# Optimization experiments

Measured on AMD Instinct MI355X. Metric: run time of the kernel, lower is better.

## Reference

```python
import jax, jax.numpy as jnp
import numpy as np

# Quantum circuit math: each wire starts in |0>, gets RX(x_i) (encoder), then a
# single-qubit, the n-wire state is a product state and each wire's <Z> is
# analytically cos(theta_i) * cos(x_i):
#   RX(x)|0> = [cos(x/2), -i sin(x/2)];  after RY(th):
#   <Z> = (cos^2(th/2)-sin^2(th/2)) * (cos^2(x/2)-sin^2(x/2)) = cos(th)cos(x).
# This is exactly the math the torchquantum simulator computes, expressed in
# closed form (no 2^d_k state vector needed).

NUM_HEADS = 64


def setup_inputs() -> dict:
    key = jax.random.key(0)
    k1, k2, k3 = jax.random.split(key, 3)
    B, T, E = 4, 1024, 512
    d_k = E // NUM_HEADS  # 8 wires
    x = jax.random.normal(k1, (B, T, E), dtype=jnp.float32)
    theta = jax.random.normal(k2, (d_k,), dtype=jnp.float32)  # shared RY params (one QLayer reused across heads)
    W_combine = jax.random.normal(k3, (E, E), dtype=jnp.float32) * (E ** -0.5)
    b_combine = jnp.zeros((E,), dtype=jnp.float32)
    return {"x": x, "theta": theta, "W_combine": W_combine, "b_combine": b_combine}


def reference(x, theta, W_combine, b_combine):
    B, T, E = x.shape
    H = NUM_HEADS
    d_k = E // H
    # split heads: [B, H, T, d_k]
    xh = x.reshape(B, T, H, d_k).transpose(0, 2, 1, 3)
    # quantum layer output: per-wire PauliZ expectation = cos(theta) * cos(x)
    proj = jnp.cos(xh) * jnp.cos(theta)  # [B, H, T, d_k]
    # self-attention on quantum projections
    scale = 1.0 / (d_k ** 0.5)
    scores = jnp.einsum('bhtd,bhsd->bhts', proj, proj) * scale  # [B, H, T, T]
    probs = jax.nn.softmax(scores, axis=-1)
    # dropout is identity in eval mode
    attn = jnp.einsum('bhts,bhsd->bhtd', probs, proj)  # [B, H, T, d_k]
    out = attn.transpose(0, 2, 1, 3).reshape(B, T, E)
    return out @ W_combine.T + b_combine
```

## Files before the change

### kernel.cpp

```cpp
#include <hip/hip_runtime.h>
#include <hip/hip_bf16.h>
#include <cstdint>
#include <cstddef>

#define T_DIM 1024
#define E_DIM 512

typedef short bf16x8 __attribute__((ext_vector_type(8)));
typedef float f32x4  __attribute__((ext_vector_type(4)));

__global__ __launch_bounds__(1024)
void qattn_mfma(const float* __restrict__ x,
                const float* __restrict__ theta,
                const float* __restrict__ W,
                __hip_bfloat16* __restrict__ attn_out,
                __hip_bfloat16* __restrict__ w_bf)
{
    __shared__ __align__(16) char shraw[16384 + 20640];
    auto projA = (__hip_bfloat16 (*)[8])(shraw);
    auto projT = (__hip_bfloat16 (*)[1032])(shraw + 16384);

    const int head = blockIdx.x;
    const int b    = head >> 6;
    const int h    = head & 63;
    const int tid  = threadIdx.x;
    const int lane = tid & 63;
    const int wv   = tid >> 6;
    const int rlo  = lane & 15;
    const int quad = lane >> 4;

    {
        const int gid = head * 1024 + tid;
        if (gid < 65536) {
            const float4 v = *(const float4*)(W + gid * 4);
            alignas(8) __hip_bfloat16 ob[4] = {
                __float2bfloat16(v.x), __float2bfloat16(v.y),
                __float2bfloat16(v.z), __float2bfloat16(v.w)};
            *(uint2*)(w_bf + gid * 4) = *(const uint2*)ob;
        }
    }

    const float SA2 = 8.0804315f;
    float ctT[8], ctA[8];
#pragma unroll
    for (int d = 0; d < 8; ++d) {
        ctT[d] = __cosf(theta[d]);
        ctA[d] = ctT[d] * SA2;
    }

    const float* xb = x + (size_t)b * T_DIM * E_DIM + h * 8;
    {
        const int r = tid;
        const float4 v0 = *(const float4*)(xb + (size_t)r * E_DIM);
        const float4 v1 = *(const float4*)(xb + (size_t)r * E_DIM + 4);
        float pr[8] = {v0.x, v0.y, v0.z, v0.w, v1.x, v1.y, v1.z, v1.w};
        alignas(16) __hip_bfloat16 ra[8];
#pragma unroll
        for (int d = 0; d < 8; ++d) {
            const float c = __cosf(pr[d]);
            ra[d] = __float2bfloat16(c * ctA[d]);
            projT[d][r] = __float2bfloat16(c * ctT[d]);
        }
        *(uint4*)&projA[r][0] = *(const uint4*)ra;
        projT[8][r] = __ushort_as_bfloat16((unsigned short)0x3f80);
        projT[9][r] = __ushort_as_bfloat16((unsigned short)0);
    }
    __syncthreads();

    const bf16x8 z8 = {};

    const float MAGIC = 8404858.0f;
    const f32x4 cinit = {MAGIC, MAGIC, MAGIC, MAGIC};

    const int q0 = wv * 64;
    bf16x8 bq[4];
#pragma unroll
    for (int tl = 0; tl < 4; ++tl)
        bq[tl] = (quad == 0) ? *(const bf16x8*)&projA[q0 + tl * 16 + rlo][0]
                             : z8;

    f32x4 nacc[4] = {};

    const __hip_bfloat16* kabase =
        (quad == 0) ? &projA[rlo][0] : &projA[0][0];
    const int bvrow = (rlo < 8) ? rlo : ((rlo == 8) ? 8 : 9);
    const __hip_bfloat16* bvbase = &projT[bvrow][quad * 4];

#pragma unroll
    for (int kc = 0; kc < 32; ++kc) {
        const int key0 = kc * 32;
        const bf16x8 ka0 = *(const bf16x8*)(kabase + (size_t)key0 * 8);
        const bf16x8 ka1 = *(const bf16x8*)(kabase + (size_t)(key0 + 16) * 8);
        union { uint2 u[2]; bf16x8 v; } uu;
        uu.u[0] = *(const uint2*)(bvbase + key0);
        uu.u[1] = *(const uint2*)(bvbase + key0 + 16);
        const bf16x8 bv = uu.v;

        f32x4 s0[4], s1[4];
#pragma unroll
        for (int tl = 0; tl < 4; ++tl) {
            s0[tl] = __builtin_amdgcn_mfma_f32_16x16x32_bf16(
                ka0, bq[tl], cinit, 0, 0, 0);
            s1[tl] = __builtin_amdgcn_mfma_f32_16x16x32_bf16(
                ka1, bq[tl], cinit, 0, 0, 0);
        }

#pragma unroll
        for (int tl = 0; tl < 4; ++tl) {
            union { f32x4 f; uint32_t u[4]; } a0, a1;
            a0.f = s0[tl];
            a1.f = s1[tl];
            union { uint32_t u[4]; bf16x8 v; } pk;
            pk.u[0] = __builtin_amdgcn_perm(a0.u[1], a0.u[0], 0x05040100u);
            pk.u[1] = __builtin_amdgcn_perm(a0.u[3], a0.u[2], 0x05040100u);
            pk.u[2] = __builtin_amdgcn_perm(a1.u[1], a1.u[0], 0x05040100u);
            pk.u[3] = __builtin_amdgcn_perm(a1.u[3], a1.u[2], 0x05040100u);
            nacc[tl] = __builtin_amdgcn_mfma_f32_16x16x32_bf16(
                pk.v, bv, nacc[tl], 0, 0, 0);
        }
    }

    const int denSrc = (lane & 48) | 8;
#pragma unroll
    for (int tl = 0; tl < 4; ++tl) {
#pragma unroll
        for (int r = 0; r < 4; ++r) {
            const float den = __shfl(nacc[tl][r], denSrc);
            const float inv = __builtin_amdgcn_rcpf(den);
            if (rlo < 8) {
                const int trow = q0 + tl * 16 + quad * 4 + r;
                attn_out[(size_t)(b * T_DIM + trow) * E_DIM + h * 8 + rlo] =
                    __float2bfloat16(nacc[tl][r] * inv);
            }
        }
    }
}

#define BM 128
#define BN 64
#define BK 64

__global__ __launch_bounds__(256, 2)
void combine_gemm(const __hip_bfloat16* __restrict__ A,
                  const __hip_bfloat16* __restrict__ Wb,
                  const float* __restrict__ bias,
                  float* __restrict__ out)
{
    __shared__ __hip_bfloat16 As[BM][BK];
    __shared__ __hip_bfloat16 Bs[BN][BK];

    const int tid  = threadIdx.x;
    const int lane = tid & 63;
    const int wave = tid >> 6;
    const int bm   = blockIdx.x;
    const int bn   = blockIdx.y;
    const int wm   = (wave & 1) * 64;
    const int wn   = (wave >> 1) * 32;
    const int rlo  = lane & 15;
    const int quad = lane >> 4;

    f32x4 acc[4][2] = {};

    for (int k0 = 0; k0 < E_DIM; k0 += BK) {
        if (k0) __syncthreads();
#pragma unroll
        for (int p = 0; p < 4; ++p) {
            const int c   = p * 256 + tid;
            const int row = c >> 3;
            const int kcs = c & 7;
            const int kc  = kcs ^ (row & 7);
            const __hip_bfloat16* gA =
                A + (size_t)(bm * BM + row) * E_DIM + k0 + kc * 8;
            char* lA = (char*)As + (size_t)(p * 256 + wave * 64) * 16;
            __builtin_amdgcn_global_load_lds(
                (const __attribute__((address_space(1))) void*)gA,
                (__attribute__((address_space(3))) void*)lA, 16, 0, 0);
        }
#pragma unroll
        for (int p = 0; p < 2; ++p) {
            const int c   = p * 256 + tid;
            const int row = c >> 3;
            const int kcs = c & 7;
            const int kc  = kcs ^ (row & 7);
            const __hip_bfloat16* gW =
                Wb + (size_t)(bn * BN + row) * E_DIM + k0 + kc * 8;
            char* lB = (char*)Bs + (size_t)(p * 256 + wave * 64) * 16;
            __builtin_amdgcn_global_load_lds(
                (const __attribute__((address_space(1))) void*)gW,
                (__attribute__((address_space(3))) void*)lB, 16, 0, 0);
        }
        __syncthreads();

#pragma unroll
        for (int ks = 0; ks < 2; ++ks) {
            const int kci  = ks * 4 + quad;
            const int koff = (kci ^ (rlo & 7)) * 8;
            bf16x8 af[4], bf[2];
#pragma unroll
            for (int i = 0; i < 4; ++i)
                af[i] = *(const bf16x8*)&As[wm + i * 16 + rlo][koff];
#pragma unroll
            for (int j = 0; j < 2; ++j)
                bf[j] = *(const bf16x8*)&Bs[wn + j * 16 + rlo][koff];
#pragma unroll
            for (int i = 0; i < 4; ++i)
#pragma unroll
                for (int j = 0; j < 2; ++j)
                    acc[i][j] = __builtin_amdgcn_mfma_f32_16x16x32_bf16(
                        af[i], bf[j], acc[i][j], 0, 0, 0);
        }
    }

    const int row0 = bm * BM + wm;
    const int col0 = bn * BN + wn;
#pragma unroll
    for (int j = 0; j < 2; ++j) {
        const int col = col0 + j * 16 + rlo;
        const float bv = bias[col];
#pragma unroll
        for (int i = 0; i < 4; ++i) {
            const int rbase = row0 + i * 16 + quad * 4;
#pragma unroll
            for (int r = 0; r < 4; ++r)
                out[(size_t)(rbase + r) * E_DIM + col] = acc[i][j][r] + bv;
        }
    }
}

extern "C" void kernel_launch(void* const* d_in, const int* in_sizes, int n_in,
                              void* d_out, int out_size, void* d_ws,
                              size_t ws_size, hipStream_t stream)
{
    const float* x     = (const float*)d_in[0];
    const float* theta = (const float*)d_in[1];
    const float* W     = (const float*)d_in[2];
    const float* bias  = (const float*)d_in[3];
    float* out = (float*)d_out;

    __hip_bfloat16* attn_bf = (__hip_bfloat16*)d_ws;
    __hip_bfloat16* w_bf    = (__hip_bfloat16*)((char*)d_ws + 4u * 1024u * 1024u);

    hipLaunchKernelGGL(qattn_mfma, dim3(256), dim3(1024), 0, stream,
                       x, theta, W, attn_bf, w_bf);
    hipLaunchKernelGGL(combine_gemm, dim3(32, 8), dim3(256), 0, stream,
                       attn_bf, w_bf, bias, out);
}
```

Baseline: 93.49 us.

## Switch attention MFMAs from 16x16x32 to 32x32x16 tiles

Rewrites the attention inner loop to use 32x32x16 bf16 MFMA instructions instead of 16x16x32. Each wave now handles two 32-query tiles with one key fragment load per 32-key chunk. The score-to-PV bf16 packing and the output row mapping are reworked for the 32x32 accumulator layout. The goal is fewer MFMA issues and fewer LDS loads per chunk. In exchange, each tile holds larger 16-float accumulators, which raises register pressure, and the zero-padded K dimension still wastes half of each score MFMA.

```diff
diff --git a/kernel.cpp b/kernel.cpp
--- a/kernel.cpp
+++ b/kernel.cpp
@@ -8,6 +8,7 @@
 
 typedef short bf16x8 __attribute__((ext_vector_type(8)));
 typedef float f32x4  __attribute__((ext_vector_type(4)));
+typedef float f32x16 __attribute__((ext_vector_type(16)));
 
 __global__ __launch_bounds__(1024)
 void qattn_mfma(const float* __restrict__ x,
@@ -26,8 +27,8 @@
     const int tid  = threadIdx.x;
     const int lane = tid & 63;
     const int wv   = tid >> 6;
-    const int rlo  = lane & 15;
-    const int quad = lane >> 4;
+    const int l31  = lane & 31;
+    const int hf   = lane >> 5;
 
     {
         const int gid = head * 1024 + tid;
@@ -70,67 +71,68 @@
     const bf16x8 z8 = {};
 
     const float MAGIC = 8404858.0f;
-    const f32x4 cinit = {MAGIC, MAGIC, MAGIC, MAGIC};
+    f32x16 cinit;
+#pragma unroll
+    for (int i = 0; i < 16; ++i) cinit[i] = MAGIC;
 
     const int q0 = wv * 64;
-    bf16x8 bq[4];
-#pragma unroll
-    for (int tl = 0; tl < 4; ++tl)
-        bq[tl] = (quad == 0) ? *(const bf16x8*)&projA[q0 + tl * 16 + rlo][0]
-                             : z8;
-
-    f32x4 nacc[4] = {};
+    bf16x8 bq[2];
+#pragma unroll
+    for (int qt = 0; qt < 2; ++qt)
+        bq[qt] = (hf == 0) ? *(const bf16x8*)&projA[q0 + qt * 32 + l31][0]
+                           : z8;
+
+    f32x16 nacc[2] = {};
 
     const __hip_bfloat16* kabase =
-        (quad == 0) ? &projA[rlo][0] : &projA[0][0];
-    const int bvrow = (rlo < 8) ? rlo : ((rlo == 8) ? 8 : 9);
-    const __hip_bfloat16* bvbase = &projT[bvrow][quad * 4];
+        (hf == 0) ? &projA[l31][0] : &projA[0][0];
+    const int bvrow = (l31 < 8) ? l31 : ((l31 == 8) ? 8 : 9);
+    const __hip_bfloat16* bvbase = &projT[bvrow][hf * 4];
 
 #pragma unroll
     for (int kc = 0; kc < 32; ++kc) {
         const int key0 = kc * 32;
-        const bf16x8 ka0 = *(const bf16x8*)(kabase + (size_t)key0 * 8);
-        const bf16x8 ka1 = *(const bf16x8*)(kabase + (size_t)(key0 + 16) * 8);
-        union { uint2 u[2]; bf16x8 v; } uu;
-        uu.u[0] = *(const uint2*)(bvbase + key0);
-        uu.u[1] = *(const uint2*)(bvbase + key0 + 16);
-        const bf16x8 bv = uu.v;
-
-        f32x4 s0[4], s1[4];
-#pragma unroll
-        for (int tl = 0; tl < 4; ++tl) {
-            s0[tl] = __builtin_amdgcn_mfma_f32_16x16x32_bf16(
-                ka0, bq[tl], cinit, 0, 0, 0);
-            s1[tl] = __builtin_amdgcn_mfma_f32_16x16x32_bf16(
-                ka1, bq[tl], cinit, 0, 0, 0);
-        }
-
-#pragma unroll
-        for (int tl = 0; tl < 4; ++tl) {
-            union { f32x4 f; uint32_t u[4]; } a0, a1;
-            a0.f = s0[tl];
-            a1.f = s1[tl];
-            union { uint32_t u[4]; bf16x8 v; } pk;
-            pk.u[0] = __builtin_amdgcn_perm(a0.u[1], a0.u[0], 0x05040100u);
-            pk.u[1] = __builtin_amdgcn_perm(a0.u[3], a0.u[2], 0x05040100u);
-            pk.u[2] = __builtin_amdgcn_perm(a1.u[1], a1.u[0], 0x05040100u);
-            pk.u[3] = __builtin_amdgcn_perm(a1.u[3], a1.u[2], 0x05040100u);
-            nacc[tl] = __builtin_amdgcn_mfma_f32_16x16x32_bf16(
-                pk.v, bv, nacc[tl], 0, 0, 0);
-        }
-    }
-
-    const int denSrc = (lane & 48) | 8;
-#pragma unroll
-    for (int tl = 0; tl < 4; ++tl) {
-#pragma unroll
-        for (int r = 0; r < 4; ++r) {
-            const float den = __shfl(nacc[tl][r], denSrc);
+        const bf16x8 ka = *(const bf16x8*)(kabase + (size_t)key0 * 8);
+
+        union { uint2 u[2]; bf16x8 v; } bA, bB;
+        bA.u[0] = *(const uint2*)(bvbase + key0);
+        bA.u[1] = *(const uint2*)(bvbase + key0 + 8);
+        bB.u[0] = *(const uint2*)(bvbase + key0 + 16);
+        bB.u[1] = *(const uint2*)(bvbase + key0 + 24);
+
+#pragma unroll
+        for (int qt = 0; qt < 2; ++qt) {
+            const f32x16 s = __builtin_amdgcn_mfma_f32_32x32x16_bf16(
+                ka, bq[qt], cinit, 0, 0, 0);
+
+            union { f32x16 f; uint32_t u[16]; } a;
+            a.f = s;
+            union { uint32_t u[4]; bf16x8 v; } pA, pB;
+#pragma unroll
+            for (int i = 0; i < 4; ++i) {
+                pA.u[i] = __builtin_amdgcn_perm(a.u[2 * i + 1], a.u[2 * i],
+                                                0x05040100u);
+                pB.u[i] = __builtin_amdgcn_perm(a.u[8 + 2 * i + 1],
+                                                a.u[8 + 2 * i], 0x05040100u);
+            }
+            nacc[qt] = __builtin_amdgcn_mfma_f32_32x32x16_bf16(
+                pA.v, bA.v, nacc[qt], 0, 0, 0);
+            nacc[qt] = __builtin_amdgcn_mfma_f32_32x32x16_bf16(
+                pB.v, bB.v, nacc[qt], 0, 0, 0);
+        }
+    }
+
+    const int denSrc = (lane & 32) | 8;
+#pragma unroll
+    for (int qt = 0; qt < 2; ++qt) {
+#pragma unroll
+        for (int r = 0; r < 16; ++r) {
+            const float den = __shfl(nacc[qt][r], denSrc);
             const float inv = __builtin_amdgcn_rcpf(den);
-            if (rlo < 8) {
-                const int trow = q0 + tl * 16 + quad * 4 + r;
-                attn_out[(size_t)(b * T_DIM + trow) * E_DIM + h * 8 + rlo] =
-                    __float2bfloat16(nacc[tl][r] * inv);
+            if (l31 < 8) {
+                const int qrow = q0 + qt * 32 + (r & 3) + 8 * (r >> 2) + 4 * hf;
+                attn_out[(size_t)(b * T_DIM + qrow) * E_DIM + h * 8 + l31] =
+                    __float2bfloat16(nacc[qt][r] * inv);
             }
         }
     }
```

Measured after the change: 95.60 us. 1.02x slower.
